# Kernel tuning notes

Measured on AMD Instinct MI355X. Metric: run time of the kernel, lower is better.

Reference implementation:

```python
import jax, jax.numpy as jnp
import numpy as np

R = 1.1
SCALE = 100.0
BUMP_STEPS = 32
NUM_THETAS = 32
NUM_FEATURES = 128
N_NODES = 200000
NUM_GRAPHS = 128


def setup_inputs() -> dict:
    key = jax.random.key(0)
    k1, k2, k3 = jax.random.split(key, 3)
    x = jax.random.normal(k1, (N_NODES, NUM_FEATURES), dtype=jnp.float32)
    batch = jnp.sort(jax.random.randint(k2, (N_NODES,), 0, NUM_GRAPHS, dtype=jnp.int64))
    v = jax.random.uniform(k3, (NUM_THETAS, NUM_FEATURES), dtype=jnp.float32) - 0.5
    return {"x": x, "batch": batch, "num_graphs": NUM_GRAPHS, "v": v}


def reference(x, batch, num_graphs, v):
    # nh: node heights along each direction theta -> [N, T]
    nh = x @ v.T
    # linspace over filtration values -> [S]
    lin = jnp.linspace(-R, R, BUMP_STEPS, dtype=nh.dtype)
    # bump: sigmoid difference; second point is the constant pad value R
    # ecc: [N, S, T]  (node-major so segment_sum reduces the leading axis)
    ecc = (jax.nn.sigmoid(SCALE * (lin[None, :, None] - nh[:, None, :]))
           - jax.nn.sigmoid(SCALE * (lin - R))[None, :, None])
    # scatter-add per graph label -> [ng, S, T] == index_add over dim1 then movedim(0,1)
    ect = jax.ops.segment_sum(ecc, batch, num_segments=num_graphs)
    return ect
```

## Files before the change

### kernel.cpp

```cpp
#include <hip/hip_runtime.h>
#include <hip/hip_bf16.h>
#include <math.h>

#define N_NODES 200000
#define NF 128
#define NT 32
#define NS 32
#define NG 128
#define ATILE 64
#define NTILES 30
#define VSTRIDE 136
#define HPAD 33

typedef short bf16x8 __attribute__((ext_vector_type(8)));
typedef float floatx4 __attribute__((ext_vector_type(4)));

__device__ __forceinline__ float rcp_fast(float x) { return __builtin_amdgcn_rcpf(x); }

__device__ __forceinline__ unsigned short bf16_bits(float f) {
    __hip_bfloat16 h = __float2bfloat16(f);
    unsigned short u; __builtin_memcpy(&u, &h, 2); return u;
}
__device__ __forceinline__ float bf16_val(unsigned short u) {
    unsigned v = (unsigned)u << 16; float f; __builtin_memcpy(&f, &v, 4); return f;
}
__device__ __forceinline__ void split1(float f, unsigned short& h, unsigned short& l) {
    h = bf16_bits(f);
    l = bf16_bits(f - bf16_val(h));
}

__device__ __forceinline__ void split8(float4 a, float4 b, bf16x8& h8, bf16x8& l8) {
    unsigned short h[8], l[8];
    split1(a.x, h[0], l[0]); split1(a.y, h[1], l[1]);
    split1(a.z, h[2], l[2]); split1(a.w, h[3], l[3]);
    split1(b.x, h[4], l[4]); split1(b.y, h[5], l[5]);
    split1(b.z, h[6], l[6]); split1(b.w, h[7], l[7]);
    h8 = (bf16x8){(short)h[0],(short)h[1],(short)h[2],(short)h[3],
                  (short)h[4],(short)h[5],(short)h[6],(short)h[7]};
    l8 = (bf16x8){(short)l[0],(short)l[1],(short)l[2],(short)l[3],
                  (short)l[4],(short)l[5],(short)l[6],(short)l[7]};
}

__device__ __forceinline__ void deposit(float* corr, int b, float z, float Lw, float C1) {
    float s0f = ceilf(z - 1.0f);
    int   s0  = (int)s0f;
    float e0  = __builtin_amdgcn_exp2f(Lw * (z - s0f));
    float e1  = e0 * C1;
    float f0  = rcp_fast(1.0f + e0);
    float f1  = rcp_fast(1.0f + e1);
    atomicAdd(&corr[b + max(s0, 0)], f0);
    int sB = s0 + 1; if (sB < 32) atomicAdd(&corr[b + sB], f1 - f0);
    int sC = s0 + 2; if (sC < 32) atomicAdd(&corr[b + sC], 1.0f - f1);
}

__global__ __launch_bounds__(256)
void graph_starts(const int* __restrict__ batch, int* __restrict__ starts) {
    int i = blockIdx.x * 256 + threadIdx.x;
    if (i >= N_NODES) return;
    int b    = batch[i];
    int prev = (i == 0) ? -1 : batch[i - 1];
    for (int g = prev + 1; g <= b; ++g) starts[g] = i;
    if (i == N_NODES - 1)
        for (int g = b + 1; g <= NG; ++g) starts[g] = N_NODES;
}

__global__ __launch_bounds__(256)
void vprep(const float* __restrict__ v,
           unsigned short* __restrict__ vth,
           unsigned short* __restrict__ vtl)
{
    const int tid = threadIdx.x;
    #pragma unroll
    for (int j = 0; j < 4; ++j) {
        int idx4 = tid * 4 + j;
        float4 val = ((const float4*)v)[idx4];
        unsigned short h0,h1,h2,h3,l0,l1,l2,l3;
        split1(val.x, h0, l0); split1(val.y, h1, l1);
        split1(val.z, h2, l2); split1(val.w, h3, l3);
        uint2 hh, ll;
        hh.x = (unsigned)h0 | ((unsigned)h1 << 16); hh.y = (unsigned)h2 | ((unsigned)h3 << 16);
        ll.x = (unsigned)l0 | ((unsigned)l1 << 16); ll.y = (unsigned)l2 | ((unsigned)l3 << 16);
        *(uint2*)&vth[idx4 * 4] = hh;
        *(uint2*)&vtl[idx4 * 4] = ll;
    }
}

__global__ __launch_bounds__(256, 6)
void ect_tile(const float* __restrict__ x,
              const float* __restrict__ v,
              const int* __restrict__ starts,
              const unsigned short* __restrict__ vth,
              const unsigned short* __restrict__ vtl,
              float* __restrict__ partials,
              float* __restrict__ out,
              int use_ws)
{
    __shared__ __align__(16) unsigned short vh[NT * VSTRIDE];
    __shared__ __align__(16) unsigned short vl[NT * VSTRIDE];
    __shared__ float corr[NT * HPAD];

    const int tid  = threadIdx.x;
    const int t    = blockIdx.x;
    const int g    = blockIdx.y;
    const int w    = tid >> 6;
    const int lane = tid & 63;
    const int mrow = lane & 15;
    const int quad = lane >> 4;

    const int start = starts[g];
    const int count = starts[g + 1] - start;
    const int slot  = g * NTILES + t;

    if (t * ATILE >= count) {
        if (use_ws) {
            float4 z4 = {0.f, 0.f, 0.f, 0.f};
            *(float4*)&partials[(size_t)slot * 1024 + tid * 4] = z4;
        }
        return;
    }
    const int base   = start + t * ATILE;
    const int nvalid = min(ATILE, count - t * ATILE);

    const int gi = min(base + w * 16 + mrow, N_NODES - 1);
    const float* __restrict__ xrow = x + (size_t)gi * NF + quad * 8;
    float4 xa[8];
    #pragma unroll
    for (int slice = 0; slice < 4; ++slice) {
        xa[2 * slice]     = *(const float4*)&xrow[slice * 32];
        xa[2 * slice + 1] = *(const float4*)&xrow[slice * 32 + 4];
    }

    if (use_ws) {
        #pragma unroll
        for (int j = 0; j < 4; ++j) {
            int idx4 = j * 256 + tid;
            int row  = idx4 >> 5;
            int f4   = idx4 & 31;
            *(uint2*)&vh[row * VSTRIDE + f4 * 4] = *(const uint2*)&vth[idx4 * 4];
            *(uint2*)&vl[row * VSTRIDE + f4 * 4] = *(const uint2*)&vtl[idx4 * 4];
        }
    } else {
        #pragma unroll
        for (int j = 0; j < 4; ++j) {
            int idx4 = j * 256 + tid;
            int row  = idx4 >> 5;
            int f4   = idx4 & 31;
            float4 val = *(const float4*)&v[(size_t)row * NF + f4 * 4];
            unsigned short h0,h1,h2,h3,l0,l1,l2,l3;
            split1(val.x, h0, l0); split1(val.y, h1, l1);
            split1(val.z, h2, l2); split1(val.w, h3, l3);
            uint2 hh, ll;
            hh.x = (unsigned)h0 | ((unsigned)h1 << 16); hh.y = (unsigned)h2 | ((unsigned)h3 << 16);
            ll.x = (unsigned)l0 | ((unsigned)l1 << 16); ll.y = (unsigned)l2 | ((unsigned)l3 << 16);
            *(uint2*)&vh[row * VSTRIDE + f4 * 4] = hh;
            *(uint2*)&vl[row * VSTRIDE + f4 * 4] = ll;
        }
    }
    for (int i = tid; i < NT * HPAD; i += 256) corr[i] = 0.0f;

    bf16x8 ah[4], al[4];
    #pragma unroll
    for (int slice = 0; slice < 4; ++slice)
        split8(xa[2 * slice], xa[2 * slice + 1], ah[slice], al[slice]);
    __syncthreads();

    const int b0base = mrow * VSTRIDE + quad * 8;
    const int b1base = (16 + mrow) * VSTRIDE + quad * 8;

    floatx4 acc0 = {0.f, 0.f, 0.f, 0.f};
    floatx4 acc1 = {0.f, 0.f, 0.f, 0.f};
    #pragma unroll
    for (int slice = 0; slice < 4; ++slice) {
        bf16x8 bh0 = *(bf16x8*)&vh[b0base + slice * 32];
        bf16x8 bl0 = *(bf16x8*)&vl[b0base + slice * 32];
        bf16x8 bh1 = *(bf16x8*)&vh[b1base + slice * 32];
        bf16x8 bl1 = *(bf16x8*)&vl[b1base + slice * 32];
        acc0 = __builtin_amdgcn_mfma_f32_16x16x32_bf16(ah[slice], bh0, acc0, 0, 0, 0);
        acc0 = __builtin_amdgcn_mfma_f32_16x16x32_bf16(ah[slice], bl0, acc0, 0, 0, 0);
        acc0 = __builtin_amdgcn_mfma_f32_16x16x32_bf16(al[slice], bh0, acc0, 0, 0, 0);
        acc1 = __builtin_amdgcn_mfma_f32_16x16x32_bf16(ah[slice], bh1, acc1, 0, 0, 0);
        acc1 = __builtin_amdgcn_mfma_f32_16x16x32_bf16(ah[slice], bl1, acc1, 0, 0, 0);
        acc1 = __builtin_amdgcn_mfma_f32_16x16x32_bf16(al[slice], bh1, acc1, 0, 0, 0);
    }

    const float inv_dlin = 14.090909090909092f;
    const float Lw       = 10.23848093f;
    const float dlin     = 2.2f / 31.0f;
    const float L        = 144.26950408889634f;
    const float C1       = 8.2777115e-04f;

    const int c0base = mrow * HPAD;
    const int c1base = (16 + mrow) * HPAD;

    float c0 = 0.f, c1 = 0.f;
    const int nloc = w * 16 + quad * 4;
    #pragma unroll
    for (int reg = 0; reg < 4; ++reg) {
        if (nloc + reg < nvalid) {
            {
                float z = fmaf(acc0[reg], inv_dlin, 15.5f);
                if (z <= -1.0f)      c0 += 1.0f;
                else if (z < 32.0f)  deposit(corr, c0base, z, Lw, C1);
            }
            {
                float z = fmaf(acc1[reg], inv_dlin, 15.5f);
                if (z <= -1.0f)      c1 += 1.0f;
                else if (z < 32.0f)  deposit(corr, c1base, z, Lw, C1);
            }
        }
    }
    if (c0 != 0.f) atomicAdd(&corr[c0base], c0);
    if (c1 != 0.f) atomicAdd(&corr[c1base], c1);
    __syncthreads();

    {
        const int grp = tid >> 5;
        const int sc  = tid & 31;
        for (int row = grp; row < NT; row += 8) {
            float val = corr[row * HPAD + sc];
            #pragma unroll
            for (int d = 1; d < 32; d <<= 1) {
                float nbr = __shfl_up(val, d, 32);
                if (sc >= d) val += nbr;
            }
            corr[row * HPAD + sc] = val;
        }
    }
    __syncthreads();

    const float cnt  = (float)nvalid;
    const int   s    = tid >> 3;
    const int   ft0  = (tid & 7) * 4;
    const float lin_s = -1.1f + (float)s * dlin;
    const float cs    = rcp_fast(1.0f + __builtin_amdgcn_exp2f(L * (1.1f - lin_s)));
    float4 r;
    r.x = corr[(ft0 + 0) * HPAD + s] - cnt * cs;
    r.y = corr[(ft0 + 1) * HPAD + s] - cnt * cs;
    r.z = corr[(ft0 + 2) * HPAD + s] - cnt * cs;
    r.w = corr[(ft0 + 3) * HPAD + s] - cnt * cs;
    if (use_ws) {
        *(float4*)&partials[(size_t)slot * 1024 + tid * 4] = r;
    } else {
        float* o = out + (size_t)g * (NS * NT) + tid * 4;
        atomicAdd(&o[0], r.x); atomicAdd(&o[1], r.y);
        atomicAdd(&o[2], r.z); atomicAdd(&o[3], r.w);
    }
}

__global__ __launch_bounds__(256)
void reduce_partials(const float* __restrict__ partials, float* __restrict__ out) {
    const int g   = blockIdx.x;
    const int tid = threadIdx.x;
    const float4* p4 = (const float4*)partials;
    float4 acc = {0.f, 0.f, 0.f, 0.f};
    #pragma unroll
    for (int t = 0; t < NTILES; ++t) {
        float4 v = p4[(size_t)(g * NTILES + t) * 256 + tid];
        acc.x += v.x; acc.y += v.y; acc.z += v.z; acc.w += v.w;
    }
    ((float4*)out)[(size_t)g * 256 + tid] = acc;
}

extern "C" void kernel_launch(void* const* d_in, const int* in_sizes, int n_in,
                              void* d_out, int out_size, void* d_ws, size_t ws_size,
                              hipStream_t stream) {
    const float* x     = (const float*)d_in[0];
    const int*   batch = (const int*)d_in[1];
    const float* v     = (const float*)d_in[3];
    float*       out   = (float*)d_out;

    int*            starts   = (int*)d_ws;
    unsigned short* vth      = (unsigned short*)((char*)d_ws + 1024);
    unsigned short* vtl      = (unsigned short*)((char*)d_ws + 1024 + 8192);
    float*          partials = (float*)((char*)d_ws + 1024 + 16384);
    const size_t need = 1024 + 16384 + (size_t)NG * NTILES * 1024 * sizeof(float);
    const int use_ws  = (ws_size >= need) ? 1 : 0;

    hipMemsetAsync(d_out, 0, (size_t)out_size * sizeof(float), stream);
    graph_starts<<<dim3((N_NODES + 255) / 256), dim3(256), 0, stream>>>(batch, starts);
    if (use_ws)
        vprep<<<dim3(1), dim3(256), 0, stream>>>(v, vth, vtl);
    ect_tile<<<dim3(NTILES, NG), dim3(256), 0, stream>>>(x, v, starts, vth, vtl,
                                                         partials, out, use_ws);
    if (use_ws)
        reduce_partials<<<dim3(NG), dim3(256), 0, stream>>>(partials, out);
}
```

Measured before the change: 173.6 us.

## XOR-swizzle shared memory, fuse prep kernels, drop memset, raise occupancy

Replaces the padded shared-memory layouts for the bf16 direction matrix and the correction histogram with XOR-swizzled unpadded layouts to avoid bank conflicts. The vprep kernel is merged into the graph_starts kernel, and the output memset is skipped when the workspace path is used. The launch-bounds occupancy hint goes from 6 to 8 blocks, and half the x loads are deferred to reduce register pressure. These changes cut launch count and LDS conflicts, at the cost of more index arithmetic and tighter register limits.

New measurement: 175.0 us. Within noise of the previous version (+0.8%).

```diff
diff --git a/kernel.cpp b/kernel.cpp
--- a/kernel.cpp
+++ b/kernel.cpp
@@ -9,8 +9,6 @@
 #define NG 128
 #define ATILE 64
 #define NTILES 30
-#define VSTRIDE 136
-#define HPAD 33
 
 typedef short bf16x8 __attribute__((ext_vector_type(8)));
 typedef float floatx4 __attribute__((ext_vector_type(4)));
@@ -28,7 +26,6 @@
     h = bf16_bits(f);
     l = bf16_bits(f - bf16_val(h));
 }
-
 __device__ __forceinline__ void split8(float4 a, float4 b, bf16x8& h8, bf16x8& l8) {
     unsigned short h[8], l[8];
     split1(a.x, h[0], l[0]); split1(a.y, h[1], l[1]);
@@ -41,20 +38,43 @@
                   (short)l[4],(short)l[5],(short)l[6],(short)l[7]};
 }
 
-__device__ __forceinline__ void deposit(float* corr, int b, float z, float Lw, float C1) {
+__device__ __forceinline__ void deposit(float* corr, int t, float z, float Lw, float C1) {
     float s0f = ceilf(z - 1.0f);
     int   s0  = (int)s0f;
     float e0  = __builtin_amdgcn_exp2f(Lw * (z - s0f));
     float e1  = e0 * C1;
     float f0  = rcp_fast(1.0f + e0);
     float f1  = rcp_fast(1.0f + e1);
-    atomicAdd(&corr[b + max(s0, 0)], f0);
-    int sB = s0 + 1; if (sB < 32) atomicAdd(&corr[b + sB], f1 - f0);
-    int sC = s0 + 2; if (sC < 32) atomicAdd(&corr[b + sC], 1.0f - f1);
+    int tb = t * 32;
+    atomicAdd(&corr[tb + (max(s0, 0) ^ t)], f0);
+    int sB = s0 + 1; if (sB < 32) atomicAdd(&corr[tb + (sB ^ t)], f1 - f0);
+    int sC = s0 + 2; if (sC < 32) atomicAdd(&corr[tb + (sC ^ t)], 1.0f - f1);
 }
 
 __global__ __launch_bounds__(256)
-void graph_starts(const int* __restrict__ batch, int* __restrict__ starts) {
+void starts_vprep(const int* __restrict__ batch, int* __restrict__ starts,
+                  const float* __restrict__ v,
+                  unsigned short* __restrict__ vth, unsigned short* __restrict__ vtl,
+                  int do_vprep)
+{
+    if (blockIdx.x == gridDim.x - 1) {
+        if (!do_vprep) return;
+        const int tid = threadIdx.x;
+        #pragma unroll
+        for (int j = 0; j < 4; ++j) {
+            int idx4 = tid * 4 + j;
+            float4 val = ((const float4*)v)[idx4];
+            unsigned short h0,h1,h2,h3,l0,l1,l2,l3;
+            split1(val.x, h0, l0); split1(val.y, h1, l1);
+            split1(val.z, h2, l2); split1(val.w, h3, l3);
+            uint2 hh, ll;
+            hh.x = (unsigned)h0 | ((unsigned)h1 << 16); hh.y = (unsigned)h2 | ((unsigned)h3 << 16);
+            ll.x = (unsigned)l0 | ((unsigned)l1 << 16); ll.y = (unsigned)l2 | ((unsigned)l3 << 16);
+            *(uint2*)&vth[idx4 * 4] = hh;
+            *(uint2*)&vtl[idx4 * 4] = ll;
+        }
+        return;
+    }
     int i = blockIdx.x * 256 + threadIdx.x;
     if (i >= N_NODES) return;
     int b    = batch[i];
@@ -64,28 +84,7 @@
         for (int g = b + 1; g <= NG; ++g) starts[g] = N_NODES;
 }
 
-__global__ __launch_bounds__(256)
-void vprep(const float* __restrict__ v,
-           unsigned short* __restrict__ vth,
-           unsigned short* __restrict__ vtl)
-{
-    const int tid = threadIdx.x;
-    #pragma unroll
-    for (int j = 0; j < 4; ++j) {
-        int idx4 = tid * 4 + j;
-        float4 val = ((const float4*)v)[idx4];
-        unsigned short h0,h1,h2,h3,l0,l1,l2,l3;
-        split1(val.x, h0, l0); split1(val.y, h1, l1);
-        split1(val.z, h2, l2); split1(val.w, h3, l3);
-        uint2 hh, ll;
-        hh.x = (unsigned)h0 | ((unsigned)h1 << 16); hh.y = (unsigned)h2 | ((unsigned)h3 << 16);
-        ll.x = (unsigned)l0 | ((unsigned)l1 << 16); ll.y = (unsigned)l2 | ((unsigned)l3 << 16);
-        *(uint2*)&vth[idx4 * 4] = hh;
-        *(uint2*)&vtl[idx4 * 4] = ll;
-    }
-}
-
-__global__ __launch_bounds__(256, 6)
+__global__ __launch_bounds__(256, 8)
 void ect_tile(const float* __restrict__ x,
               const float* __restrict__ v,
               const int* __restrict__ starts,
@@ -95,9 +94,9 @@
               float* __restrict__ out,
               int use_ws)
 {
-    __shared__ __align__(16) unsigned short vh[NT * VSTRIDE];
-    __shared__ __align__(16) unsigned short vl[NT * VSTRIDE];
-    __shared__ float corr[NT * HPAD];
+    __shared__ __align__(16) unsigned short vh[NT * 128];
+    __shared__ __align__(16) unsigned short vl[NT * 128];
+    __shared__ float corr[NT * 32];
 
     const int tid  = threadIdx.x;
     const int t    = blockIdx.x;
@@ -123,64 +122,73 @@
 
     const int gi = min(base + w * 16 + mrow, N_NODES - 1);
     const float* __restrict__ xrow = x + (size_t)gi * NF + quad * 8;
-    float4 xa[8];
-    #pragma unroll
-    for (int slice = 0; slice < 4; ++slice) {
-        xa[2 * slice]     = *(const float4*)&xrow[slice * 32];
-        xa[2 * slice + 1] = *(const float4*)&xrow[slice * 32 + 4];
-    }
+    float4 xa0 = *(const float4*)&xrow[0];
+    float4 xa1 = *(const float4*)&xrow[4];
+    float4 xa2 = *(const float4*)&xrow[32];
+    float4 xa3 = *(const float4*)&xrow[36];
 
     if (use_ws) {
         #pragma unroll
-        for (int j = 0; j < 4; ++j) {
-            int idx4 = j * 256 + tid;
-            int row  = idx4 >> 5;
-            int f4   = idx4 & 31;
-            *(uint2*)&vh[row * VSTRIDE + f4 * 4] = *(const uint2*)&vth[idx4 * 4];
-            *(uint2*)&vl[row * VSTRIDE + f4 * 4] = *(const uint2*)&vtl[idx4 * 4];
+        for (int j = 0; j < 2; ++j) {
+            int u    = j * 256 + tid;
+            int row  = u >> 4;
+            int s16p = (u & 15) ^ (row & 15);
+            *(uint4*)&vh[row * 128 + s16p * 8] = *(const uint4*)&vth[u * 8];
+            *(uint4*)&vl[row * 128 + s16p * 8] = *(const uint4*)&vtl[u * 8];
         }
     } else {
         #pragma unroll
         for (int j = 0; j < 4; ++j) {
             int idx4 = j * 256 + tid;
             int row  = idx4 >> 5;
-            int f4   = idx4 & 31;
-            float4 val = *(const float4*)&v[(size_t)row * NF + f4 * 4];
+            int col8 = idx4 & 31;
+            int col8p = (((col8 >> 1) ^ (row & 15)) << 1) | (col8 & 1);
+            float4 val = *(const float4*)&v[(size_t)row * NF + col8 * 4];
             unsigned short h0,h1,h2,h3,l0,l1,l2,l3;
             split1(val.x, h0, l0); split1(val.y, h1, l1);
             split1(val.z, h2, l2); split1(val.w, h3, l3);
             uint2 hh, ll;
             hh.x = (unsigned)h0 | ((unsigned)h1 << 16); hh.y = (unsigned)h2 | ((unsigned)h3 << 16);
             ll.x = (unsigned)l0 | ((unsigned)l1 << 16); ll.y = (unsigned)l2 | ((unsigned)l3 << 16);
-            *(uint2*)&vh[row * VSTRIDE + f4 * 4] = hh;
-            *(uint2*)&vl[row * VSTRIDE + f4 * 4] = ll;
-        }
-    }
-    for (int i = tid; i < NT * HPAD; i += 256) corr[i] = 0.0f;
-
-    bf16x8 ah[4], al[4];
-    #pragma unroll
-    for (int slice = 0; slice < 4; ++slice)
-        split8(xa[2 * slice], xa[2 * slice + 1], ah[slice], al[slice]);
+            *(uint2*)&vh[row * 128 + col8p * 4] = hh;
+            *(uint2*)&vl[row * 128 + col8p * 4] = ll;
+        }
+    }
+    #pragma unroll
+    for (int i = tid; i < NT * 32; i += 256) corr[i] = 0.0f;
+
+    bf16x8 ah0, al0, ah1, al1;
+    split8(xa0, xa1, ah0, al0);
+    split8(xa2, xa3, ah1, al1);
+    float4 xb0 = *(const float4*)&xrow[64];
+    float4 xb1 = *(const float4*)&xrow[68];
+    float4 xb2 = *(const float4*)&xrow[96];
+    float4 xb3 = *(const float4*)&xrow[100];
     __syncthreads();
-
-    const int b0base = mrow * VSTRIDE + quad * 8;
-    const int b1base = (16 + mrow) * VSTRIDE + quad * 8;
 
     floatx4 acc0 = {0.f, 0.f, 0.f, 0.f};
     floatx4 acc1 = {0.f, 0.f, 0.f, 0.f};
+    const int o0 = mrow * 128;
+    const int o1 = o0 + 2048;
     #pragma unroll
     for (int slice = 0; slice < 4; ++slice) {
-        bf16x8 bh0 = *(bf16x8*)&vh[b0base + slice * 32];
-        bf16x8 bl0 = *(bf16x8*)&vl[b0base + slice * 32];
-        bf16x8 bh1 = *(bf16x8*)&vh[b1base + slice * 32];
-        bf16x8 bl1 = *(bf16x8*)&vl[b1base + slice * 32];
-        acc0 = __builtin_amdgcn_mfma_f32_16x16x32_bf16(ah[slice], bh0, acc0, 0, 0, 0);
-        acc0 = __builtin_amdgcn_mfma_f32_16x16x32_bf16(ah[slice], bl0, acc0, 0, 0, 0);
-        acc0 = __builtin_amdgcn_mfma_f32_16x16x32_bf16(al[slice], bh0, acc0, 0, 0, 0);
-        acc1 = __builtin_amdgcn_mfma_f32_16x16x32_bf16(ah[slice], bh1, acc1, 0, 0, 0);
-        acc1 = __builtin_amdgcn_mfma_f32_16x16x32_bf16(ah[slice], bl1, acc1, 0, 0, 0);
-        acc1 = __builtin_amdgcn_mfma_f32_16x16x32_bf16(al[slice], bh1, acc1, 0, 0, 0);
+        if (slice == 2) {
+            split8(xb0, xb1, ah0, al0);
+            split8(xb2, xb3, ah1, al1);
+        }
+        bf16x8 a_h = (slice & 1) ? ah1 : ah0;
+        bf16x8 a_l = (slice & 1) ? al1 : al0;
+        int sp = (((quad | (slice << 2)) ^ mrow) << 3);
+        bf16x8 bh0 = *(bf16x8*)&vh[o0 + sp];
+        bf16x8 bl0 = *(bf16x8*)&vl[o0 + sp];
+        bf16x8 bh1 = *(bf16x8*)&vh[o1 + sp];
+        bf16x8 bl1 = *(bf16x8*)&vl[o1 + sp];
+        acc0 = __builtin_amdgcn_mfma_f32_16x16x32_bf16(a_h, bh0, acc0, 0, 0, 0);
+        acc0 = __builtin_amdgcn_mfma_f32_16x16x32_bf16(a_h, bl0, acc0, 0, 0, 0);
+        acc0 = __builtin_amdgcn_mfma_f32_16x16x32_bf16(a_l, bh0, acc0, 0, 0, 0);
+        acc1 = __builtin_amdgcn_mfma_f32_16x16x32_bf16(a_h, bh1, acc1, 0, 0, 0);
+        acc1 = __builtin_amdgcn_mfma_f32_16x16x32_bf16(a_h, bl1, acc1, 0, 0, 0);
+        acc1 = __builtin_amdgcn_mfma_f32_16x16x32_bf16(a_l, bh1, acc1, 0, 0, 0);
     }
 
     const float inv_dlin = 14.090909090909092f;
@@ -189,9 +197,6 @@
     const float L        = 144.26950408889634f;
     const float C1       = 8.2777115e-04f;
 
-    const int c0base = mrow * HPAD;
-    const int c1base = (16 + mrow) * HPAD;
-
     float c0 = 0.f, c1 = 0.f;
     const int nloc = w * 16 + quad * 4;
     #pragma unroll
@@ -200,30 +205,30 @@
             {
                 float z = fmaf(acc0[reg], inv_dlin, 15.5f);
                 if (z <= -1.0f)      c0 += 1.0f;
-                else if (z < 32.0f)  deposit(corr, c0base, z, Lw, C1);
+                else if (z < 32.0f)  deposit(corr, mrow, z, Lw, C1);
             }
             {
                 float z = fmaf(acc1[reg], inv_dlin, 15.5f);
                 if (z <= -1.0f)      c1 += 1.0f;
-                else if (z < 32.0f)  deposit(corr, c1base, z, Lw, C1);
+                else if (z < 32.0f)  deposit(corr, 16 + mrow, z, Lw, C1);
             }
         }
     }
-    if (c0 != 0.f) atomicAdd(&corr[c0base], c0);
-    if (c1 != 0.f) atomicAdd(&corr[c1base], c1);
+    if (c0 != 0.f) atomicAdd(&corr[mrow * 32 + (0 ^ mrow)], c0);
+    if (c1 != 0.f) atomicAdd(&corr[(16 + mrow) * 32 + (0 ^ (16 + mrow))], c1);
     __syncthreads();
 
     {
         const int grp = tid >> 5;
         const int sc  = tid & 31;
         for (int row = grp; row < NT; row += 8) {
-            float val = corr[row * HPAD + sc];
+            float val = corr[row * 32 + (sc ^ row)];
             #pragma unroll
             for (int d = 1; d < 32; d <<= 1) {
                 float nbr = __shfl_up(val, d, 32);
                 if (sc >= d) val += nbr;
             }
-            corr[row * HPAD + sc] = val;
+            corr[row * 32 + (sc ^ row)] = val;
         }
     }
     __syncthreads();
@@ -234,10 +239,10 @@
     const float lin_s = -1.1f + (float)s * dlin;
     const float cs    = rcp_fast(1.0f + __builtin_amdgcn_exp2f(L * (1.1f - lin_s)));
     float4 r;
-    r.x = corr[(ft0 + 0) * HPAD + s] - cnt * cs;
-    r.y = corr[(ft0 + 1) * HPAD + s] - cnt * cs;
-    r.z = corr[(ft0 + 2) * HPAD + s] - cnt * cs;
-    r.w = corr[(ft0 + 3) * HPAD + s] - cnt * cs;
+    r.x = corr[(ft0 + 0) * 32 + (s ^ (ft0 + 0))] - cnt * cs;
+    r.y = corr[(ft0 + 1) * 32 + (s ^ (ft0 + 1))] - cnt * cs;
+    r.z = corr[(ft0 + 2) * 32 + (s ^ (ft0 + 2))] - cnt * cs;
+    r.w = corr[(ft0 + 3) * 32 + (s ^ (ft0 + 3))] - cnt * cs;
     if (use_ws) {
         *(float4*)&partials[(size_t)slot * 1024 + tid * 4] = r;
     } else {
@@ -276,12 +281,15 @@
     const size_t need = 1024 + 16384 + (size_t)NG * NTILES * 1024 * sizeof(float);
     const int use_ws  = (ws_size >= need) ? 1 : 0;
 
-    hipMemsetAsync(d_out, 0, (size_t)out_size * sizeof(float), stream);
-    graph_starts<<<dim3((N_NODES + 255) / 256), dim3(256), 0, stream>>>(batch, starts);
-    if (use_ws)
-        vprep<<<dim3(1), dim3(256), 0, stream>>>(v, vth, vtl);
-    ect_tile<<<dim3(NTILES, NG), dim3(256), 0, stream>>>(x, v, starts, vth, vtl,
-                                                         partials, out, use_ws);
-    if (use_ws)
+    const int nsb = (N_NODES + 255) / 256 + 1;
+    starts_vprep<<<dim3(nsb), dim3(256), 0, stream>>>(batch, starts, v, vth, vtl, use_ws);
+    if (use_ws) {
+        ect_tile<<<dim3(NTILES, NG), dim3(256), 0, stream>>>(x, v, starts, vth, vtl,
+                                                             partials, out, 1);
         reduce_partials<<<dim3(NG), dim3(256), 0, stream>>>(partials, out);
-}
+    } else {
+        hipMemsetAsync(d_out, 0, (size_t)out_size * sizeof(float), stream);
+        ect_tile<<<dim3(NTILES, NG), dim3(256), 0, stream>>>(x, v, starts, vth, vtl,
+                                                             partials, out, 0);
+    }
+}
```
